# Kernel tuning notes

Measured on AMD Instinct MI355X. Metric: run time of the kernel, lower is better.

Reference implementation:

```python
import jax, jax.numpy as jnp
import numpy as np

B, SQ, SK, D, H = 4, 2048, 2048, 1024, 16
HD = D // H


def setup_inputs() -> dict:
    key = jax.random.key(0)
    ks = jax.random.split(key, 12)
    s = 1.0 / np.sqrt(D)
    return {
        "query": jax.random.normal(ks[0], (B, SQ, D), jnp.float32),
        "key": jax.random.normal(ks[1], (B, SK, D), jnp.float32),
        "value": jax.random.normal(ks[2], (B, SK, D), jnp.float32),
        "key_padding_mask": jax.random.randint(ks[3], (B, SK), 0, 2, jnp.int32),
        "Wq": jax.random.uniform(ks[4], (D, D), jnp.float32, -s, s),
        "bq": jnp.zeros((D,), jnp.float32),
        "Wk": jax.random.uniform(ks[5], (D, D), jnp.float32, -s, s),
        "bk": jnp.zeros((D,), jnp.float32),
        "Wv": jax.random.uniform(ks[6], (D, D), jnp.float32, -s, s),
        "bv": jnp.zeros((D,), jnp.float32),
        "Wo": jax.random.uniform(ks[7], (D, D), jnp.float32, -s, s),
        "bo": jnp.zeros((D,), jnp.float32),
    }


def reference(query, key, value, key_padding_mask, Wq, bq, Wk, bk, Wv, bv, Wo, bo):
    scale = HD ** -0.5
    # projections: torch Linear is x @ W.T + b
    q = (query @ Wq.T + bq).reshape(B, SQ, H, HD).transpose(0, 2, 1, 3)  # [B,H,SQ,HD]
    k = (key @ Wk.T + bk).reshape(B, SK, H, HD).transpose(0, 2, 1, 3)    # [B,H,SK,HD]
    v = (value @ Wv.T + bv).reshape(B, SK, H, HD).transpose(0, 2, 1, 3)  # [B,H,SK,HD]
    scores = jnp.einsum("bhqd,bhkd->bhqk", q, k) * scale                  # [B,H,SQ,SK]
    mask = key_padding_mask[:, None, None, :] != 0                        # True = keep
    scores = jnp.where(mask, scores, -jnp.inf)
    attn = jax.nn.softmax(scores, axis=-1)
    # dropout is identity at inference (eval mode)
    out = jnp.einsum("bhqk,bhkd->bhqd", attn, v)                          # [B,H,SQ,HD]
    out = out.transpose(0, 2, 1, 3).reshape(B, SQ, D)
    return out @ Wo.T + bo
```

## Files before the change

kernel.cpp:

```cpp
#include <hip/hip_runtime.h>


typedef __bf16 bf16_t;
typedef __attribute__((ext_vector_type(4))) __bf16 bf16x4;
typedef __attribute__((ext_vector_type(8))) __bf16 bf16x8;
typedef __attribute__((ext_vector_type(4))) float f32x4;

#define MFMA16(a, b, c) __builtin_amdgcn_mfma_f32_16x16x32_bf16(a, b, c, 0, 0, 0)

__device__ __forceinline__ void gl_lds16(const void* g, void* l) {
  __builtin_amdgcn_global_load_lds(
      (const __attribute__((address_space(1))) unsigned int*)g,
      (__attribute__((address_space(3))) unsigned int*)l, 16, 0, 0);
}

__global__ void wconv_kernel(const float* __restrict__ Wq, const float* __restrict__ Wk,
                             const float* __restrict__ Wv, const float* __restrict__ Wo,
                             bf16_t* __restrict__ out) {
  const int m = blockIdx.y;
  const float* src = (m == 0) ? Wq : (m == 1) ? Wk : (m == 2) ? Wv : Wo;
  bf16_t* dst = out + (size_t)m * (1024 * 1024);
  const int idx = (blockIdx.x * 256 + threadIdx.x) * 4;
  float4 v = *(const float4*)(src + idx);
  bf16x4 pk;
  pk[0] = (bf16_t)v.x; pk[1] = (bf16_t)v.y; pk[2] = (bf16_t)v.z; pk[3] = (bf16_t)v.w;
  *(bf16x4*)(dst + idx) = pk;
}

template <bool A_F32>
__global__ __launch_bounds__(256, 2) void gemm_kernel(
    const void* __restrict__ Aptr, const bf16_t* __restrict__ Bw,
    const float* __restrict__ bias, void* __restrict__ outp, const int out_mode) {
  __shared__ __align__(16) bf16_t As[2][16 * 512];
  __shared__ __align__(16) bf16_t Bs[2][16 * 512];

  const int tid = threadIdx.x;
  const int lane = tid & 63, wave = tid >> 6;
  const int fm = lane & 15, quad = lane >> 4;
  const int wr = wave >> 1, wc = wave & 1;
  const int m0 = blockIdx.x * 128, n0 = blockIdx.y * 128;

  f32x4 acc[4][4];
#pragma unroll
  for (int i = 0; i < 4; ++i)
#pragma unroll
    for (int j = 0; j < 4; ++j) acc[i][j] = f32x4{0.f, 0.f, 0.f, 0.f};

  auto stage = [&](int ks, int buf) {
    const int k0 = ks * 64;
    if constexpr (A_F32) {
      const float* A = (const float*)Aptr;
#pragma unroll
      for (int it = 0; it < 4; ++it) {
        const int fid = wave * 4 + it;
        const int row = (fid >> 1) * 16 + fm;
        const int col = (fid & 1) * 32 + quad * 8;
        const float* src = A + (size_t)(m0 + row) * 1024 + k0 + col;
        float4 v0 = *(const float4*)src, v1 = *(const float4*)(src + 4);
        bf16x8 pk;
        pk[0] = (bf16_t)v0.x; pk[1] = (bf16_t)v0.y; pk[2] = (bf16_t)v0.z; pk[3] = (bf16_t)v0.w;
        pk[4] = (bf16_t)v1.x; pk[5] = (bf16_t)v1.y; pk[6] = (bf16_t)v1.z; pk[7] = (bf16_t)v1.w;
        *(bf16x8*)(As[buf] + fid * 512 + lane * 8) = pk;
      }
    } else {
      const bf16_t* A = (const bf16_t*)Aptr;
#pragma unroll
      for (int it = 0; it < 4; ++it) {
        const int fid = wave * 4 + it;
        const int row = (fid >> 1) * 16 + fm;
        const int col = (fid & 1) * 32 + quad * 8;
        gl_lds16(A + (size_t)(m0 + row) * 1024 + k0 + col, As[buf] + fid * 512);
      }
    }
#pragma unroll
    for (int it = 0; it < 4; ++it) {
      const int fid = wave * 4 + it;
      const int row = (fid >> 1) * 16 + fm;
      const int col = (fid & 1) * 32 + quad * 8;
      gl_lds16(Bw + (size_t)(n0 + row) * 1024 + k0 + col, Bs[buf] + fid * 512);
    }
  };

  stage(0, 0);
  for (int ks = 0; ks < 16; ++ks) {
    __syncthreads();
    if (ks + 1 < 16) stage(ks + 1, (ks + 1) & 1);
    const bf16_t* Ab = As[ks & 1];
    const bf16_t* Bb = Bs[ks & 1];
#pragma unroll
    for (int u = 0; u < 2; ++u) {
      bf16x8 af[4], bfr[4];
#pragma unroll
      for (int i = 0; i < 4; ++i)
        af[i] = *(const bf16x8*)(Ab + ((4 * wr + i) * 2 + u) * 512 + lane * 8);
#pragma unroll
      for (int j = 0; j < 4; ++j)
        bfr[j] = *(const bf16x8*)(Bb + ((4 * wc + j) * 2 + u) * 512 + lane * 8);
#pragma unroll
      for (int i = 0; i < 4; ++i)
#pragma unroll
        for (int j = 0; j < 4; ++j) acc[i][j] = MFMA16(af[i], bfr[j], acc[i][j]);
    }
  }

  float bval[4];
#pragma unroll
  for (int j = 0; j < 4; ++j) bval[j] = bias[n0 + wc * 64 + j * 16 + fm];

#pragma unroll
  for (int i = 0; i < 4; ++i) {
#pragma unroll
    for (int j = 0; j < 4; ++j) {
      const int col = n0 + wc * 64 + j * 16 + fm;
#pragma unroll
      for (int r = 0; r < 4; ++r) {
        const int row = m0 + wr * 64 + i * 16 + quad * 4 + r;
        const float v = acc[i][j][r] + bval[j];
        if (out_mode == 2) {
          ((float*)outp)[(size_t)row * 1024 + col] = v;
        } else if (out_mode == 0) {
          ((bf16_t*)outp)[(size_t)row * 1024 + col] = (bf16_t)v;
        } else {
          const int bb = row >> 11, sk = row & 2047;
          const int tt = sk >> 7, L128 = sk & 127;
          const int c = L128 >> 5, hf = (L128 >> 4) & 1;
          const int qd = (L128 >> 2) & 3, rr = L128 & 3;
          const int hh = col >> 6, hd = col & 63;
          const int nt = hd >> 4, fv = hd & 15;
          const size_t idx = (((size_t)(bb * 16 + hh)) << 17) + tt * 8192 +
                             (nt * 4 + c) * 512 + (qd * 16 + fv) * 8 + hf * 4 + rr;
          ((bf16_t*)outp)[idx] = (bf16_t)v;
        }
      }
    }
  }
}

__global__ __launch_bounds__(256, 2) void attn_kernel(
    const bf16_t* __restrict__ q16, const bf16_t* __restrict__ k16,
    const bf16_t* __restrict__ vt16, const int* __restrict__ mask,
    bf16_t* __restrict__ o16) {
  __shared__ __align__(16) bf16_t Kb[2][8192];
  __shared__ __align__(16) bf16_t Vb[2][8192];
  __shared__ float mbuf[2][128];
  __shared__ float lbuf[128];

  const int tid = threadIdx.x;
  const int lane = tid & 63, wave = tid >> 6;
  const int fm = lane & 15, quad = lane >> 4;
  const int qt = blockIdx.x, bh = blockIdx.y;
  const int b = bh >> 4, h = bh & 15;
  const float SC = 0.125f * 1.44269504f;

  bf16x8 aq[2][2];
#pragma unroll
  for (int i = 0; i < 2; ++i)
#pragma unroll
    for (int dc = 0; dc < 2; ++dc) {
      const int row = qt * 128 + (2 * wave + i) * 16 + fm;
      aq[i][dc] = *(const bf16x8*)(q16 + ((size_t)(b * 2048 + row)) * 1024 + h * 64 +
                                   dc * 32 + quad * 8);
    }

  auto stageKV = [&](int t, int buf) {
    const bf16_t* kb = k16 + ((size_t)(b * 2048 + t * 128)) * 1024 + h * 64;
#pragma unroll
    for (int s = 0; s < 4; ++s) {
      const int fid = wave * 4 + s;
      const int row = (fid >> 1) * 16 + fm;
      const int col = (fid & 1) * 32 + quad * 8;
      gl_lds16(kb + (size_t)row * 1024 + col, Kb[buf] + fid * 512);
    }
    const bf16_t* vbase = vt16 + ((size_t)bh << 17) + t * 8192;
#pragma unroll
    for (int s = 0; s < 4; ++s) {
      const int fid = wave * 4 + s;
      gl_lds16(vbase + fid * 512 + lane * 8, Vb[buf] + fid * 512);
    }
    if (tid < 128) mbuf[buf][tid] = mask[b * 2048 + t * 128 + tid] ? 0.0f : -1e30f;
  };

  f32x4 oacc[2][4];
#pragma unroll
  for (int i = 0; i < 2; ++i)
#pragma unroll
    for (int n = 0; n < 4; ++n) oacc[i][n] = f32x4{0.f, 0.f, 0.f, 0.f};
  float lrow[2] = {0.f, 0.f};

  stageKV(0, 0);
  for (int t = 0; t < 16; ++t) {
    __syncthreads();
    if (t + 1 < 16) stageKV(t + 1, (t + 1) & 1);
    const bf16_t* K = Kb[t & 1];
    const bf16_t* V = Vb[t & 1];
    const float* mb = mbuf[t & 1];

    f32x4 sacc[2][8];
#pragma unroll
    for (int i = 0; i < 2; ++i)
#pragma unroll
      for (int j = 0; j < 8; ++j) sacc[i][j] = f32x4{0.f, 0.f, 0.f, 0.f};
#pragma unroll
    for (int j = 0; j < 8; ++j) {
#pragma unroll
      for (int dc = 0; dc < 2; ++dc) {
        bf16x8 kf = *(const bf16x8*)(K + (j * 2 + dc) * 512 + lane * 8);
        sacc[0][j] = MFMA16(kf, aq[0][dc], sacc[0][j]);
        sacc[1][j] = MFMA16(kf, aq[1][dc], sacc[1][j]);
      }
    }

#pragma unroll
    for (int j = 0; j < 8; ++j) {
      f32x4 md = *(const f32x4*)&mb[j * 16 + quad * 4];
#pragma unroll
      for (int i = 0; i < 2; ++i) {
#pragma unroll
        for (int r = 0; r < 4; ++r) {
          const float p = __builtin_amdgcn_exp2f(fmaf(sacc[i][j][r], SC, md[r]));
          sacc[i][j][r] = p;
          lrow[i] += p;
        }
      }
    }

#pragma unroll
    for (int c = 0; c < 4; ++c) {
      bf16x8 pf[2];
#pragma unroll
      for (int i = 0; i < 2; ++i) {
#pragma unroll
        for (int r = 0; r < 4; ++r) {
          pf[i][r] = (bf16_t)sacc[i][2 * c][r];
          pf[i][4 + r] = (bf16_t)sacc[i][2 * c + 1][r];
        }
      }
#pragma unroll
      for (int n = 0; n < 4; ++n) {
        bf16x8 vv = *(const bf16x8*)(V + (n * 4 + c) * 512 + lane * 8);
        oacc[0][n] = MFMA16(pf[0], vv, oacc[0][n]);
        oacc[1][n] = MFMA16(pf[1], vv, oacc[1][n]);
      }
    }
  }

#pragma unroll
  for (int i = 0; i < 2; ++i) {
    float l = lrow[i];
    l += __shfl_xor(l, 16);
    l += __shfl_xor(l, 32);
    if (quad == 0) lbuf[wave * 32 + i * 16 + fm] = l;
  }
  __syncthreads();
#pragma unroll
  for (int i = 0; i < 2; ++i) {
    f32x4 lv = *(const f32x4*)&lbuf[wave * 32 + i * 16 + quad * 4];
#pragma unroll
    for (int r = 0; r < 4; ++r) {
      const float inv = 1.0f / lv[r];
      const int row = qt * 128 + wave * 32 + i * 16 + quad * 4 + r;
#pragma unroll
      for (int n = 0; n < 4; ++n) {
        o16[((size_t)(b * 2048 + row)) * 1024 + h * 64 + n * 16 + fm] =
            (bf16_t)(oacc[i][n][r] * inv);
      }
    }
  }
}

extern "C" void kernel_launch(void* const* d_in, const int* in_sizes, int n_in,
                              void* d_out, int out_size, void* d_ws, size_t ws_size,
                              hipStream_t stream) {
  const float* query = (const float*)d_in[0];
  const float* key   = (const float*)d_in[1];
  const float* value = (const float*)d_in[2];
  const int* mask    = (const int*)d_in[3];
  const float* Wq = (const float*)d_in[4];
  const float* bq = (const float*)d_in[5];
  const float* Wk = (const float*)d_in[6];
  const float* bk = (const float*)d_in[7];
  const float* Wv = (const float*)d_in[8];
  const float* bv = (const float*)d_in[9];
  const float* Wo = (const float*)d_in[10];
  const float* bo = (const float*)d_in[11];

  char* ws = (char*)d_ws;
  bf16_t* W16  = (bf16_t*)ws;
  bf16_t* q16  = (bf16_t*)(ws + (size_t)8 * 1024 * 1024);
  bf16_t* k16  = q16 + 8388608;
  bf16_t* vt16 = k16 + 8388608;
  bf16_t* o16  = vt16 + 8388608;

  wconv_kernel<<<dim3(1024, 4), 256, 0, stream>>>(Wq, Wk, Wv, Wo, W16);
  gemm_kernel<true><<<dim3(64, 8), 256, 0, stream>>>(query, W16,           bq, q16,  0);
  gemm_kernel<true><<<dim3(64, 8), 256, 0, stream>>>(key,   W16 + 1048576, bk, k16,  0);
  gemm_kernel<true><<<dim3(64, 8), 256, 0, stream>>>(value, W16 + 2097152, bv, vt16, 1);
  attn_kernel<<<dim3(16, 64), 256, 0, stream>>>(q16, k16, vt16, mask, o16);
  gemm_kernel<false><<<dim3(64, 8), 256, 0, stream>>>(o16, W16 + 3145728, bo, d_out, 2);
}
```

Baseline: 418.9 us.

## Pre-convert inputs to bf16 in one pass and remap attention blocks per XCD

Adds one conversion kernel that casts query, key, value and all four weights to bf16 in a single launch. The projection GEMMs can then use the bf16-input path instead of converting fp32 activations while loading tiles. The attention grid is also remapped so that blocks sharing a batch-head land on the same XCD, which should improve L2 reuse of K/V. This costs an extra full read and write of the activations and needs more workspace; when the workspace is too small the old path runs instead.

```diff
diff --git a/kernel.cpp b/kernel.cpp
--- a/kernel.cpp
+++ b/kernel.cpp
@@ -24,6 +24,33 @@
   float4 v = *(const float4*)(src + idx);
   bf16x4 pk;
   pk[0] = (bf16_t)v.x; pk[1] = (bf16_t)v.y; pk[2] = (bf16_t)v.z; pk[3] = (bf16_t)v.w;
+  *(bf16x4*)(dst + idx) = pk;
+}
+
+__global__ void conv_kernel(const float* __restrict__ q, const float* __restrict__ k,
+                            const float* __restrict__ v, const float* __restrict__ Wq,
+                            const float* __restrict__ Wk, const float* __restrict__ Wv,
+                            const float* __restrict__ Wo, bf16_t* __restrict__ q16,
+                            bf16_t* __restrict__ k16, bf16_t* __restrict__ v16,
+                            bf16_t* __restrict__ W16) {
+  const int y = blockIdx.y;
+  const float* src;
+  bf16_t* dst;
+  size_t idx;
+  if (y < 3) {
+    src = (y == 0) ? q : (y == 1) ? k : v;
+    dst = (y == 0) ? q16 : (y == 1) ? k16 : v16;
+    idx = ((size_t)blockIdx.x * 256 + threadIdx.x) * 4;
+  } else {
+    if (blockIdx.x >= 4096) return;
+    const int m = blockIdx.x >> 10;
+    src = (m == 0) ? Wq : (m == 1) ? Wk : (m == 2) ? Wv : Wo;
+    dst = W16 + ((size_t)m << 20);
+    idx = (((size_t)(blockIdx.x & 1023)) * 256 + threadIdx.x) * 4;
+  }
+  float4 w = *(const float4*)(src + idx);
+  bf16x4 pk;
+  pk[0] = (bf16_t)w.x; pk[1] = (bf16_t)w.y; pk[2] = (bf16_t)w.z; pk[3] = (bf16_t)w.w;
   *(bf16x4*)(dst + idx) = pk;
 }
 
@@ -148,7 +175,10 @@
   const int tid = threadIdx.x;
   const int lane = tid & 63, wave = tid >> 6;
   const int fm = lane & 15, quad = lane >> 4;
-  const int qt = blockIdx.x, bh = blockIdx.y;
+  const int lin = blockIdx.y * 16 + blockIdx.x;
+  const int xcd = lin & 7, slot = lin >> 3;
+  const int qt = slot & 15;
+  const int bh = ((slot >> 4) << 3) + xcd;
   const int b = bh >> 4, h = bh & 15;
   const float SC = 0.125f * 1.44269504f;
 
@@ -284,17 +314,32 @@
   const float* Wo = (const float*)d_in[10];
   const float* bo = (const float*)d_in[11];
 
+  const size_t MB = 1024 * 1024;
   char* ws = (char*)d_ws;
   bf16_t* W16  = (bf16_t*)ws;
-  bf16_t* q16  = (bf16_t*)(ws + (size_t)8 * 1024 * 1024);
-  bf16_t* k16  = q16 + 8388608;
-  bf16_t* vt16 = k16 + 8388608;
-  bf16_t* o16  = vt16 + 8388608;
-
-  wconv_kernel<<<dim3(1024, 4), 256, 0, stream>>>(Wq, Wk, Wv, Wo, W16);
-  gemm_kernel<true><<<dim3(64, 8), 256, 0, stream>>>(query, W16,           bq, q16,  0);
-  gemm_kernel<true><<<dim3(64, 8), 256, 0, stream>>>(key,   W16 + 1048576, bk, k16,  0);
-  gemm_kernel<true><<<dim3(64, 8), 256, 0, stream>>>(value, W16 + 2097152, bv, vt16, 1);
-  attn_kernel<<<dim3(16, 64), 256, 0, stream>>>(q16, k16, vt16, mask, o16);
-  gemm_kernel<false><<<dim3(64, 8), 256, 0, stream>>>(o16, W16 + 3145728, bo, d_out, 2);
-}
+  bf16_t* q16  = (bf16_t*)(ws + 8 * MB);
+  bf16_t* k16  = (bf16_t*)(ws + 24 * MB);
+  bf16_t* vt16 = (bf16_t*)(ws + 40 * MB);
+  bf16_t* o16  = (bf16_t*)(ws + 56 * MB);
+
+  if (ws_size >= 104 * MB) {
+    bf16_t* qin16 = o16;
+    bf16_t* kin16 = (bf16_t*)(ws + 72 * MB);
+    bf16_t* vin16 = (bf16_t*)(ws + 88 * MB);
+
+    conv_kernel<<<dim3(8192, 4), 256, 0, stream>>>(query, key, value, Wq, Wk, Wv, Wo,
+                                                   qin16, kin16, vin16, W16);
+    gemm_kernel<false><<<dim3(64, 8), 256, 0, stream>>>(qin16, W16,           bq, q16,  0);
+    gemm_kernel<false><<<dim3(64, 8), 256, 0, stream>>>(kin16, W16 + 1048576, bk, k16,  0);
+    gemm_kernel<false><<<dim3(64, 8), 256, 0, stream>>>(vin16, W16 + 2097152, bv, vt16, 1);
+    attn_kernel<<<dim3(16, 64), 256, 0, stream>>>(q16, k16, vt16, mask, o16);
+    gemm_kernel<false><<<dim3(64, 8), 256, 0, stream>>>(o16, W16 + 3145728, bo, d_out, 2);
+  } else {
+    wconv_kernel<<<dim3(1024, 4), 256, 0, stream>>>(Wq, Wk, Wv, Wo, W16);
+    gemm_kernel<true><<<dim3(64, 8), 256, 0, stream>>>(query, W16,           bq, q16,  0);
+    gemm_kernel<true><<<dim3(64, 8), 256, 0, stream>>>(key,   W16 + 1048576, bk, k16,  0);
+    gemm_kernel<true><<<dim3(64, 8), 256, 0, stream>>>(value, W16 + 2097152, bv, vt16, 1);
+    attn_kernel<<<dim3(16, 64), 256, 0, stream>>>(q16, k16, vt16, mask, o16);
+    gemm_kernel<false><<<dim3(64, 8), 256, 0, stream>>>(o16, W16 + 3145728, bo, d_out, 2);
+  }
+}
```

Result: no change. 420.8 us (+0.5%).

## Pre-convert fp32 inputs to bf16 and remap attention blocks across XCDs

Applied to the files above, without the earlier changes.

Adds a separate elementwise kernel that converts each fp32 activation input to bf16 in a scratch buffer. The projection GEMMs can then always use the asynchronous global-to-LDS load path, replacing register-staged fp32 loads and in-loop conversion. The attention kernel also remaps block indices so that all query tiles of one batch-head land on the same XCD, aiming for better L2 reuse of K/V. The cost is three extra kernel launches and an additional round trip through memory for the 48MB of fp32 inputs.

```diff
diff --git a/kernel.cpp b/kernel.cpp
--- a/kernel.cpp
+++ b/kernel.cpp
@@ -27,9 +27,16 @@
   *(bf16x4*)(dst + idx) = pk;
 }
 
-template <bool A_F32>
+__global__ void iconv_kernel(const float* __restrict__ src, bf16_t* __restrict__ dst) {
+  const size_t idx = ((size_t)blockIdx.x * 256 + threadIdx.x) * 4;
+  float4 v = *(const float4*)(src + idx);
+  bf16x4 pk;
+  pk[0] = (bf16_t)v.x; pk[1] = (bf16_t)v.y; pk[2] = (bf16_t)v.z; pk[3] = (bf16_t)v.w;
+  *(bf16x4*)(dst + idx) = pk;
+}
+
 __global__ __launch_bounds__(256, 2) void gemm_kernel(
-    const void* __restrict__ Aptr, const bf16_t* __restrict__ Bw,
+    const bf16_t* __restrict__ A, const bf16_t* __restrict__ Bw,
     const float* __restrict__ bias, void* __restrict__ outp, const int out_mode) {
   __shared__ __align__(16) bf16_t As[2][16 * 512];
   __shared__ __align__(16) bf16_t Bs[2][16 * 512];
@@ -48,29 +55,12 @@
 
   auto stage = [&](int ks, int buf) {
     const int k0 = ks * 64;
-    if constexpr (A_F32) {
-      const float* A = (const float*)Aptr;
-#pragma unroll
-      for (int it = 0; it < 4; ++it) {
-        const int fid = wave * 4 + it;
-        const int row = (fid >> 1) * 16 + fm;
-        const int col = (fid & 1) * 32 + quad * 8;
-        const float* src = A + (size_t)(m0 + row) * 1024 + k0 + col;
-        float4 v0 = *(const float4*)src, v1 = *(const float4*)(src + 4);
-        bf16x8 pk;
-        pk[0] = (bf16_t)v0.x; pk[1] = (bf16_t)v0.y; pk[2] = (bf16_t)v0.z; pk[3] = (bf16_t)v0.w;
-        pk[4] = (bf16_t)v1.x; pk[5] = (bf16_t)v1.y; pk[6] = (bf16_t)v1.z; pk[7] = (bf16_t)v1.w;
-        *(bf16x8*)(As[buf] + fid * 512 + lane * 8) = pk;
-      }
-    } else {
-      const bf16_t* A = (const bf16_t*)Aptr;
-#pragma unroll
-      for (int it = 0; it < 4; ++it) {
-        const int fid = wave * 4 + it;
-        const int row = (fid >> 1) * 16 + fm;
-        const int col = (fid & 1) * 32 + quad * 8;
-        gl_lds16(A + (size_t)(m0 + row) * 1024 + k0 + col, As[buf] + fid * 512);
-      }
+#pragma unroll
+    for (int it = 0; it < 4; ++it) {
+      const int fid = wave * 4 + it;
+      const int row = (fid >> 1) * 16 + fm;
+      const int col = (fid & 1) * 32 + quad * 8;
+      gl_lds16(A + (size_t)(m0 + row) * 1024 + k0 + col, As[buf] + fid * 512);
     }
 #pragma unroll
     for (int it = 0; it < 4; ++it) {
@@ -148,7 +138,10 @@
   const int tid = threadIdx.x;
   const int lane = tid & 63, wave = tid >> 6;
   const int fm = lane & 15, quad = lane >> 4;
-  const int qt = blockIdx.x, bh = blockIdx.y;
+  const int lin = blockIdx.y * 16 + blockIdx.x;
+  const int xcd = lin & 7, slot = lin >> 3;
+  const int qt = slot & 15;
+  const int bh = ((slot >> 4) << 3) + xcd;
   const int b = bh >> 4, h = bh & 15;
   const float SC = 0.125f * 1.44269504f;
 
@@ -284,17 +277,26 @@
   const float* Wo = (const float*)d_in[10];
   const float* bo = (const float*)d_in[11];
 
+  const size_t MB = 1024 * 1024;
   char* ws = (char*)d_ws;
-  bf16_t* W16  = (bf16_t*)ws;
-  bf16_t* q16  = (bf16_t*)(ws + (size_t)8 * 1024 * 1024);
-  bf16_t* k16  = q16 + 8388608;
-  bf16_t* vt16 = k16 + 8388608;
-  bf16_t* o16  = vt16 + 8388608;
+  bf16_t* W16     = (bf16_t*)ws;
+  bf16_t* q16     = (bf16_t*)(ws + 8 * MB);
+  bf16_t* k16     = (bf16_t*)(ws + 24 * MB);
+  bf16_t* vt16    = (bf16_t*)(ws + 40 * MB);
+  bf16_t* scratch = (bf16_t*)(ws + 56 * MB);
 
   wconv_kernel<<<dim3(1024, 4), 256, 0, stream>>>(Wq, Wk, Wv, Wo, W16);
-  gemm_kernel<true><<<dim3(64, 8), 256, 0, stream>>>(query, W16,           bq, q16,  0);
-  gemm_kernel<true><<<dim3(64, 8), 256, 0, stream>>>(key,   W16 + 1048576, bk, k16,  0);
-  gemm_kernel<true><<<dim3(64, 8), 256, 0, stream>>>(value, W16 + 2097152, bv, vt16, 1);
-  attn_kernel<<<dim3(16, 64), 256, 0, stream>>>(q16, k16, vt16, mask, o16);
-  gemm_kernel<false><<<dim3(64, 8), 256, 0, stream>>>(o16, W16 + 3145728, bo, d_out, 2);
-}
+
+  iconv_kernel<<<8192, 256, 0, stream>>>(query, scratch);
+  gemm_kernel<<<dim3(64, 8), 256, 0, stream>>>(scratch, W16,           bq, q16,  0);
+
+  iconv_kernel<<<8192, 256, 0, stream>>>(key, scratch);
+  gemm_kernel<<<dim3(64, 8), 256, 0, stream>>>(scratch, W16 + 1048576, bk, k16,  0);
+
+  iconv_kernel<<<8192, 256, 0, stream>>>(value, scratch);
+  gemm_kernel<<<dim3(64, 8), 256, 0, stream>>>(scratch, W16 + 2097152, bv, vt16, 1);
+
+  attn_kernel<<<dim3(16, 64), 256, 0, stream>>>(q16, k16, vt16, mask, scratch);
+
+  gemm_kernel<<<dim3(64, 8), 256, 0, stream>>>(scratch, W16 + 3145728, bo, d_out, 2);
+}
```

New measurement: 433.0 us. 1.03x slower.

## Batch QKV projections into one launch, halve GEMM K-tile, remap attention blocks per XCD

Applied to the files above, without the earlier changes.

The three Q/K/V projection GEMMs are merged into one launch using blockIdx.z to select the input, weights, bias and output. The GEMM K-step drops from 64 to 32, which halves LDS use and raises the occupancy hint from 2 to 4 blocks per CU, at the cost of twice as many barrier-separated iterations. The attention kernel remaps linear block ids so that blocks landing on the same XCD share a (batch, head) pair, aiming for better L2 reuse of K/V. Together these target launch overhead, occupancy and cache locality.

```diff
diff --git a/kernel.cpp b/kernel.cpp
--- a/kernel.cpp
+++ b/kernel.cpp
@@ -28,11 +28,21 @@
 }
 
 template <bool A_F32>
-__global__ __launch_bounds__(256, 2) void gemm_kernel(
-    const void* __restrict__ Aptr, const bf16_t* __restrict__ Bw,
-    const float* __restrict__ bias, void* __restrict__ outp, const int out_mode) {
-  __shared__ __align__(16) bf16_t As[2][16 * 512];
-  __shared__ __align__(16) bf16_t Bs[2][16 * 512];
+__global__ __launch_bounds__(256, 4) void gemm_kernel(
+    const void* __restrict__ A0, const void* __restrict__ A1,
+    const void* __restrict__ A2, const bf16_t* __restrict__ Wbase,
+    const float* __restrict__ b0, const float* __restrict__ b1,
+    const float* __restrict__ b2, void* __restrict__ o0, void* __restrict__ o1,
+    void* __restrict__ o2, const int md0, const int md1, const int md2) {
+  __shared__ __align__(16) bf16_t As[2][8 * 512];
+  __shared__ __align__(16) bf16_t Bs[2][8 * 512];
+
+  const int z = blockIdx.z;
+  const void* Aptr = (z == 0) ? A0 : (z == 1) ? A1 : A2;
+  const bf16_t* Bw = Wbase + ((size_t)z << 20);
+  const float* bias = (z == 0) ? b0 : (z == 1) ? b1 : b2;
+  void* outp = (z == 0) ? o0 : (z == 1) ? o1 : o2;
+  const int out_mode = (z == 0) ? md0 : (z == 1) ? md1 : md2;
 
   const int tid = threadIdx.x;
   const int lane = tid & 63, wave = tid >> 6;
@@ -47,15 +57,13 @@
     for (int j = 0; j < 4; ++j) acc[i][j] = f32x4{0.f, 0.f, 0.f, 0.f};
 
   auto stage = [&](int ks, int buf) {
-    const int k0 = ks * 64;
+    const int k0 = ks * 32;
     if constexpr (A_F32) {
       const float* A = (const float*)Aptr;
 #pragma unroll
-      for (int it = 0; it < 4; ++it) {
-        const int fid = wave * 4 + it;
-        const int row = (fid >> 1) * 16 + fm;
-        const int col = (fid & 1) * 32 + quad * 8;
-        const float* src = A + (size_t)(m0 + row) * 1024 + k0 + col;
+      for (int it = 0; it < 2; ++it) {
+        const int fid = wave * 2 + it;
+        const float* src = A + (size_t)(m0 + fid * 16 + fm) * 1024 + k0 + quad * 8;
         float4 v0 = *(const float4*)src, v1 = *(const float4*)(src + 4);
         bf16x8 pk;
         pk[0] = (bf16_t)v0.x; pk[1] = (bf16_t)v0.y; pk[2] = (bf16_t)v0.z; pk[3] = (bf16_t)v0.w;
@@ -65,42 +73,37 @@
     } else {
       const bf16_t* A = (const bf16_t*)Aptr;
 #pragma unroll
-      for (int it = 0; it < 4; ++it) {
-        const int fid = wave * 4 + it;
-        const int row = (fid >> 1) * 16 + fm;
-        const int col = (fid & 1) * 32 + quad * 8;
-        gl_lds16(A + (size_t)(m0 + row) * 1024 + k0 + col, As[buf] + fid * 512);
-      }
-    }
-#pragma unroll
-    for (int it = 0; it < 4; ++it) {
-      const int fid = wave * 4 + it;
-      const int row = (fid >> 1) * 16 + fm;
-      const int col = (fid & 1) * 32 + quad * 8;
-      gl_lds16(Bw + (size_t)(n0 + row) * 1024 + k0 + col, Bs[buf] + fid * 512);
+      for (int it = 0; it < 2; ++it) {
+        const int fid = wave * 2 + it;
+        gl_lds16(A + (size_t)(m0 + fid * 16 + fm) * 1024 + k0 + quad * 8,
+                 As[buf] + fid * 512);
+      }
+    }
+#pragma unroll
+    for (int it = 0; it < 2; ++it) {
+      const int fid = wave * 2 + it;
+      gl_lds16(Bw + (size_t)(n0 + fid * 16 + fm) * 1024 + k0 + quad * 8,
+               Bs[buf] + fid * 512);
     }
   };
 
   stage(0, 0);
-  for (int ks = 0; ks < 16; ++ks) {
+  for (int ks = 0; ks < 32; ++ks) {
     __syncthreads();
-    if (ks + 1 < 16) stage(ks + 1, (ks + 1) & 1);
+    if (ks + 1 < 32) stage(ks + 1, (ks + 1) & 1);
     const bf16_t* Ab = As[ks & 1];
     const bf16_t* Bb = Bs[ks & 1];
-#pragma unroll
-    for (int u = 0; u < 2; ++u) {
-      bf16x8 af[4], bfr[4];
-#pragma unroll
-      for (int i = 0; i < 4; ++i)
-        af[i] = *(const bf16x8*)(Ab + ((4 * wr + i) * 2 + u) * 512 + lane * 8);
-#pragma unroll
-      for (int j = 0; j < 4; ++j)
-        bfr[j] = *(const bf16x8*)(Bb + ((4 * wc + j) * 2 + u) * 512 + lane * 8);
-#pragma unroll
-      for (int i = 0; i < 4; ++i)
-#pragma unroll
-        for (int j = 0; j < 4; ++j) acc[i][j] = MFMA16(af[i], bfr[j], acc[i][j]);
-    }
+    bf16x8 af[4], bfr[4];
+#pragma unroll
+    for (int i = 0; i < 4; ++i)
+      af[i] = *(const bf16x8*)(Ab + (4 * wr + i) * 512 + lane * 8);
+#pragma unroll
+    for (int j = 0; j < 4; ++j)
+      bfr[j] = *(const bf16x8*)(Bb + (4 * wc + j) * 512 + lane * 8);
+#pragma unroll
+    for (int i = 0; i < 4; ++i)
+#pragma unroll
+      for (int j = 0; j < 4; ++j) acc[i][j] = MFMA16(af[i], bfr[j], acc[i][j]);
   }
 
   float bval[4];
@@ -148,7 +151,10 @@
   const int tid = threadIdx.x;
   const int lane = tid & 63, wave = tid >> 6;
   const int fm = lane & 15, quad = lane >> 4;
-  const int qt = blockIdx.x, bh = blockIdx.y;
+  const int lin = blockIdx.y * 16 + blockIdx.x;
+  const int xcd = lin & 7, slot = lin >> 3;
+  const int qt = slot & 15;
+  const int bh = ((slot >> 4) << 3) + xcd;
   const int b = bh >> 4, h = bh & 15;
   const float SC = 0.125f * 1.44269504f;
 
@@ -284,17 +290,22 @@
   const float* Wo = (const float*)d_in[10];
   const float* bo = (const float*)d_in[11];
 
+  const size_t MB = 1024 * 1024;
   char* ws = (char*)d_ws;
   bf16_t* W16  = (bf16_t*)ws;
-  bf16_t* q16  = (bf16_t*)(ws + (size_t)8 * 1024 * 1024);
-  bf16_t* k16  = q16 + 8388608;
-  bf16_t* vt16 = k16 + 8388608;
-  bf16_t* o16  = vt16 + 8388608;
+  bf16_t* q16  = (bf16_t*)(ws + 8 * MB);
+  bf16_t* k16  = (bf16_t*)(ws + 24 * MB);
+  bf16_t* vt16 = (bf16_t*)(ws + 40 * MB);
+  bf16_t* o16  = (bf16_t*)(ws + 56 * MB);
 
   wconv_kernel<<<dim3(1024, 4), 256, 0, stream>>>(Wq, Wk, Wv, Wo, W16);
-  gemm_kernel<true><<<dim3(64, 8), 256, 0, stream>>>(query, W16,           bq, q16,  0);
-  gemm_kernel<true><<<dim3(64, 8), 256, 0, stream>>>(key,   W16 + 1048576, bk, k16,  0);
-  gemm_kernel<true><<<dim3(64, 8), 256, 0, stream>>>(value, W16 + 2097152, bv, vt16, 1);
+
+  gemm_kernel<true><<<dim3(64, 8, 3), 256, 0, stream>>>(
+      query, key, value, W16, bq, bk, bv, q16, k16, vt16, 0, 0, 1);
+
   attn_kernel<<<dim3(16, 64), 256, 0, stream>>>(q16, k16, vt16, mask, o16);
-  gemm_kernel<false><<<dim3(64, 8), 256, 0, stream>>>(o16, W16 + 3145728, bo, d_out, 2);
-}
+
+  gemm_kernel<false><<<dim3(64, 8, 1), 256, 0, stream>>>(
+      o16, nullptr, nullptr, W16 + 3145728, bo, nullptr, nullptr, d_out, nullptr,
+      nullptr, 2, 0, 0);
+}
```

New measurement: 409.6 us. 2.2% less time.
